# Kernel tuning notes

Measured on AMD Instinct MI355X. Metric: run time of the kernel, lower is better.

Reference implementation:

```python
import jax, jax.numpy as jnp
import numpy as np

H, W, CIN = 448, 608, 64
D = (128, 128, 1024)  # depth list from the module
SCALE = 0.02

def setup_inputs() -> dict:
    key = jax.random.key(0)
    ks = jax.random.split(key, 9)
    f32 = jnp.float32
    return {
        "x":  jax.random.normal(ks[0], (1, CIN, H, W), f32),
        "w1": jax.random.normal(ks[1], (D[0], CIN, 3, 3), f32) * SCALE,
        "b1": jax.random.normal(ks[2], (D[0],), f32) * SCALE,
        "w2": jax.random.normal(ks[3], (H, D[1], D[0]), f32) * SCALE,
        "b2": jax.random.normal(ks[4], (H, D[1]), f32) * SCALE,
        "w3": jax.random.normal(ks[5], (H, D[2], D[1]), f32) * SCALE,
        "b3": jax.random.normal(ks[6], (H, D[2]), f32) * SCALE,
        "w4": jax.random.normal(ks[7], (H, 2, D[2]), f32) * SCALE,
        "b4": jax.random.normal(ks[8], (H, 2), f32) * SCALE,
    }

def _lrelu(v):
    return jax.nn.leaky_relu(v, 0.01)  # PyTorch F.leaky_relu default slope

def reference(x, w1, b1, w2, b2, w3, b3, w4, b4):
    # stage_1: 3x3 conv, padding=1, + leaky_relu   -> [B,128,H,W]
    y = jax.lax.conv_general_dilated(
        x, w1, window_strides=(1, 1), padding='SAME',
        dimension_numbers=('NCHW', 'OIHW', 'NCHW'))
    y = _lrelu(y + b1[None, :, None, None])
    # transpose(1,2) + reshape -> grouped 1x1 convs (groups=H) == per-row GEMMs
    y = jnp.transpose(y, (0, 2, 1, 3))                      # [B,H,128,W]
    y = _lrelu(jnp.einsum('bhcw,hdc->bhdw', y, w2) + b2[None, :, :, None])
    y = _lrelu(jnp.einsum('bhcw,hdc->bhdw', y, w3) + b3[None, :, :, None])
    y = jnp.einsum('bhcw,hdc->bhdw', y, w4) + b4[None, :, :, None]  # [B,H,2,W]
    y = jnp.transpose(y, (0, 2, 1, 3))                      # [B,2,H,W]
    out = y[:, 0]
    mask = _lrelu(y[:, 1])   # mask branch      [B,H,W]
    return (out, mask)
```

## Files before the change

kernel.cpp:

```cpp
#include <hip/hip_runtime.h>

#define HH 448
#define WW 608
#define D1 128
#define D2 128
#define D3 1024
#define HWPROD (HH*WW)
#define CLW 164

typedef __bf16 bf16x8 __attribute__((ext_vector_type(8)));
typedef float  f32x4  __attribute__((ext_vector_type(4)));

__device__ inline unsigned short f2bf(float v) {
    __bf16 b = (__bf16)v;
    return __builtin_bit_cast(unsigned short, b);
}

__device__ inline bf16x8 cvt8c(const float* __restrict__ p) {
    f32x4 f0 = *reinterpret_cast<const f32x4*>(p);
    f32x4 f1 = *reinterpret_cast<const f32x4*>(p + 4);
    bf16x8 r;
    r[0]=(__bf16)f0[0]; r[1]=(__bf16)f0[1]; r[2]=(__bf16)f0[2]; r[3]=(__bf16)f0[3];
    r[4]=(__bf16)f1[0]; r[5]=(__bf16)f1[1]; r[6]=(__bf16)f1[2]; r[7]=(__bf16)f1[3];
    return r;
}

__global__ __launch_bounds__(256) void transpose_x_kernel(
    const float* __restrict__ x, unsigned short* __restrict__ xt)
{
    const int pos = blockIdx.x * 256 + threadIdx.x;
    #pragma unroll
    for (int c8 = 0; c8 < 8; ++c8) {
        bf16x8 r;
        #pragma unroll
        for (int j = 0; j < 8; ++j)
            r[j] = (__bf16)x[(size_t)(c8 * 8 + j) * HWPROD + pos];
        *reinterpret_cast<bf16x8*>(xt + (size_t)pos * 64 + c8 * 8) = r;
    }
}

__global__ __launch_bounds__(256) void convert_w1_kernel(
    const float* __restrict__ w1, unsigned short* __restrict__ w1t)
{
    const int idx = blockIdx.x * 256 + threadIdx.x;
    if (idx >= 9 * D1 * 64) return;
    const int tap = idx / (D1 * 64);
    const int rem = idx - tap * (D1 * 64);
    const int d = rem >> 6, c = rem & 63;
    w1t[idx] = f2bf(w1[(d * 64 + c) * 9 + tap]);
}

__global__ __launch_bounds__(512) void conv_kernel(
    const unsigned short* __restrict__ xt, const unsigned short* __restrict__ w1t,
    const float* __restrict__ b1, unsigned short* __restrict__ y1)
{
    __shared__ __align__(16) unsigned char lds[3 * CLW * 128];
    const int h      = blockIdx.y;
    const int wstart = blockIdx.x * 152;
    const int tid  = threadIdx.x;
    const int lane = tid & 63, wv = tid >> 6;
    const int l15 = lane & 15, lg = lane >> 4;
    const int wd = wv >> 2, wn = wv & 3;
    const int d0 = wd * 64;
    const int start = (wn < 2) ? wn * 3 : 6 + (wn - 2) * 2;
    const int cnt   = (wn < 2) ? 3 : 2;

    for (int i = 0; i < 8; ++i) {
        const int s = i * 512 + tid;
        if (s < 3 * CLW * 8) {
            const int slot = s & 7;
            const int rw   = s >> 3;
            const int ri   = rw / CLW;
            const int wl   = rw - ri * CLW;
            const int hs   = h + ri - 1;
            const int gw   = wstart + wl - 1;
            uint4 val = {0u, 0u, 0u, 0u};
            if ((unsigned)hs < (unsigned)HH && (unsigned)gw < (unsigned)WW)
                val = *reinterpret_cast<const uint4*>(xt + ((size_t)hs * WW + gw) * 64 + slot * 8);
            const int dslot = slot ^ (rw & 7);
            *reinterpret_cast<uint4*>(&lds[(size_t)rw * 128 + dslot * 16]) = val;
        }
    }
    __syncthreads();

    f32x4 acc[3][4] = {};

    #pragma unroll
    for (int tap = 0; tap < 9; ++tap) {
        const int ty = tap / 3, tx = tap - ty * 3;
        bf16x8 a[4][2];
        #pragma unroll
        for (int mf = 0; mf < 4; ++mf)
            #pragma unroll
            for (int kc = 0; kc < 2; ++kc)
                a[mf][kc] = *reinterpret_cast<const bf16x8*>(
                    w1t + ((size_t)(tap * D1 + d0 + mf * 16 + l15)) * 64 + kc * 32 + lg * 8);
        #pragma unroll
        for (int f = 0; f < 3; ++f) {
            if (f < cnt) {
                const int col = (start + f) * 16 + l15;
                const int row = ty * CLW + col + tx;
                bf16x8 b[2];
                #pragma unroll
                for (int kc = 0; kc < 2; ++kc) {
                    const int sl = (kc * 4 + lg) ^ (row & 7);
                    b[kc] = *reinterpret_cast<const bf16x8*>(&lds[(size_t)row * 128 + sl * 16]);
                }
                #pragma unroll
                for (int mf = 0; mf < 4; ++mf)
                    #pragma unroll
                    for (int kc = 0; kc < 2; ++kc)
                        acc[f][mf] = __builtin_amdgcn_mfma_f32_16x16x32_bf16(
                            a[mf][kc], b[kc], acc[f][mf], 0, 0, 0);
            }
        }
    }

    f32x4 b1v[4];
    #pragma unroll
    for (int mf = 0; mf < 4; ++mf)
        b1v[mf] = *reinterpret_cast<const f32x4*>(b1 + d0 + mf * 16 + lg * 4);

    #pragma unroll
    for (int f = 0; f < 3; ++f) {
        if (f < cnt) {
            const int wl = (start + f) * 16 + l15;
            if (wl < 152) {
                const int w = wstart + wl;
                #pragma unroll
                for (int mf = 0; mf < 4; ++mf) {
                    ushort4 o;
                    #pragma unroll
                    for (int r = 0; r < 4; ++r) {
                        float v = acc[f][mf][r] + b1v[mf][r];
                        v = fmaxf(v, 0.01f * v);
                        ((unsigned short*)&o)[r] = f2bf(v);
                    }
                    *reinterpret_cast<ushort4*>(
                        y1 + ((size_t)h * WW + w) * D1 + d0 + mf * 16 + lg * 4) = o;
                }
            }
        }
    }
}

__device__ inline void decode_pair(int bid, int& h, int& half) {
    const int s = bid & 7, j = bid >> 3;
    half = j & 1;
    h = (j >> 1) * 8 + s;
}

__global__ __launch_bounds__(512) void gemm2_kernel(
    const unsigned short* __restrict__ y1, const float* __restrict__ w2,
    const float* __restrict__ b2, unsigned short* __restrict__ y2)
{
    __shared__ __align__(16) unsigned char lds[304 * 256];
    int h, half;
    decode_pair(blockIdx.x, h, half);
    const int wstart = half * 304;
    const int tid = threadIdx.x;
    const int lane = tid & 63, wv = tid >> 6;
    const int l15 = lane & 15, lg = lane >> 4;
    const int e0 = wv * 16;

    {
        const unsigned char* src = reinterpret_cast<const unsigned char*>(
            y1 + ((size_t)h * WW + wstart) * D1);
        #pragma unroll
        for (int i = 0; i < 10; ++i) {
            const int c16 = i * 512 + tid;
            if (c16 < 304 * 16) {
                const int byte = c16 * 16;
                const int row  = byte >> 8;
                const int slot = (byte >> 4) & 15;
                uint4 val = *reinterpret_cast<const uint4*>(src + byte);
                *reinterpret_cast<uint4*>(&lds[row * 256 + ((slot ^ (row & 15)) << 4)]) = val;
            }
        }
    }

    bf16x8 a[4];
    #pragma unroll
    for (int kc = 0; kc < 4; ++kc)
        a[kc] = cvt8c(w2 + ((size_t)h * D2 + e0 + l15) * D1 + kc * 32 + lg * 8);
    f32x4 b2v = *reinterpret_cast<const f32x4*>(b2 + (size_t)h * D2 + e0 + lg * 4);

    __syncthreads();

    for (int nf = 0; nf < 19; ++nf) {
        const int wl = nf * 16 + l15;
        bf16x8 b[4];
        #pragma unroll
        for (int kc = 0; kc < 4; ++kc) {
            const int sl = (kc * 4 + lg) ^ (wl & 15);
            b[kc] = *reinterpret_cast<const bf16x8*>(&lds[(size_t)wl * 256 + sl * 16]);
        }
        f32x4 t = {};
        #pragma unroll
        for (int kc = 0; kc < 4; ++kc)
            t = __builtin_amdgcn_mfma_f32_16x16x32_bf16(a[kc], b[kc], t, 0, 0, 0);
        ushort4 o;
        #pragma unroll
        for (int r = 0; r < 4; ++r) {
            float v = t[r] + b2v[r];
            v = fmaxf(v, 0.01f * v);
            ((unsigned short*)&o)[r] = f2bf(v);
        }
        *reinterpret_cast<ushort4*>(
            y2 + ((size_t)h * WW + wstart + wl) * D2 + e0 + lg * 4) = o;
    }
}

__global__ __launch_bounds__(512) void gemm3_kernel(
    const unsigned short* __restrict__ y2, const float* __restrict__ w3,
    const float* __restrict__ b3, const float* __restrict__ w4,
    const float* __restrict__ b4, float* __restrict__ out)
{
    __shared__ __align__(16) unsigned char lds[304 * 256 + 2 * 304 * 4];
    float* pk = reinterpret_cast<float*>(&lds[304 * 256]);
    int h, half;
    decode_pair(blockIdx.x, h, half);
    const int wstart = half * 304;
    const int tid = threadIdx.x;
    const int lane = tid & 63, wv = tid >> 6;
    const int l15 = lane & 15, lg = lane >> 4;
    const int e0 = wv * 128;

    for (int i = tid; i < 2 * 304; i += 512) pk[i] = 0.f;

    {
        const unsigned char* src = reinterpret_cast<const unsigned char*>(
            y2 + ((size_t)h * WW + wstart) * D2);
        #pragma unroll
        for (int i = 0; i < 10; ++i) {
            const int c16 = i * 512 + tid;
            if (c16 < 304 * 16) {
                const int byte = c16 * 16;
                const int row  = byte >> 8;
                const int slot = (byte >> 4) & 15;
                uint4 val = *reinterpret_cast<const uint4*>(src + byte);
                *reinterpret_cast<uint4*>(&lds[row * 256 + ((slot ^ (row & 15)) << 4)]) = val;
            }
        }
    }
    __syncthreads();

    for (int ct = 0; ct < 4; ++ct) {
        const int e32 = e0 + ct * 32;
        bf16x8 a[2][4];
        #pragma unroll
        for (int mf = 0; mf < 2; ++mf)
            #pragma unroll
            for (int kc = 0; kc < 4; ++kc)
                a[mf][kc] = cvt8c(w3 + ((size_t)h * D3 + e32 + mf * 16 + l15) * D2 + kc * 32 + lg * 8);
        f32x4 b3v[2], w40[2], w41[2];
        #pragma unroll
        for (int mf = 0; mf < 2; ++mf) {
            b3v[mf] = *reinterpret_cast<const f32x4*>(b3 + (size_t)h * D3 + e32 + mf * 16 + lg * 4);
            w40[mf] = *reinterpret_cast<const f32x4*>(w4 + (size_t)h * 2 * D3 + e32 + mf * 16 + lg * 4);
            w41[mf] = *reinterpret_cast<const f32x4*>(w4 + (size_t)h * 2 * D3 + D3 + e32 + mf * 16 + lg * 4);
        }

        for (int nf = 0; nf < 19; ++nf) {
            const int wl = nf * 16 + l15;
            bf16x8 b[4];
            #pragma unroll
            for (int kc = 0; kc < 4; ++kc) {
                const int sl = (kc * 4 + lg) ^ (wl & 15);
                b[kc] = *reinterpret_cast<const bf16x8*>(&lds[(size_t)wl * 256 + sl * 16]);
            }
            float p0 = 0.f, p1 = 0.f;
            #pragma unroll
            for (int mf = 0; mf < 2; ++mf) {
                f32x4 t = {};
                #pragma unroll
                for (int kc = 0; kc < 4; ++kc)
                    t = __builtin_amdgcn_mfma_f32_16x16x32_bf16(a[mf][kc], b[kc], t, 0, 0, 0);
                #pragma unroll
                for (int r = 0; r < 4; ++r) {
                    float v = t[r] + b3v[mf][r];
                    v = fmaxf(v, 0.01f * v);
                    p0 = fmaf(w40[mf][r], v, p0);
                    p1 = fmaf(w41[mf][r], v, p1);
                }
            }
            p0 += __shfl_xor(p0, 16); p0 += __shfl_xor(p0, 32);
            p1 += __shfl_xor(p1, 16); p1 += __shfl_xor(p1, 32);
            if (lane < 16) {
                atomicAdd(&pk[wl], p0);
                atomicAdd(&pk[304 + wl], p1);
            }
        }
    }
    __syncthreads();

    const float bb0 = b4[h * 2 + 0], bb1 = b4[h * 2 + 1];
    for (int i = tid; i < 304; i += 512) {
        float s0 = pk[i] + bb0;
        float s1 = pk[304 + i] + bb1;
        out[(size_t)h * WW + wstart + i] = s0;
        out[(size_t)HWPROD + (size_t)h * WW + wstart + i] = fmaxf(s1, 0.01f * s1);
    }
}

extern "C" void kernel_launch(void* const* d_in, const int* in_sizes, int n_in,
                              void* d_out, int out_size, void* d_ws, size_t ws_size,
                              hipStream_t stream) {
    const float* x  = (const float*)d_in[0];
    const float* w1 = (const float*)d_in[1];
    const float* b1 = (const float*)d_in[2];
    const float* w2 = (const float*)d_in[3];
    const float* b2 = (const float*)d_in[4];
    const float* w3 = (const float*)d_in[5];
    const float* b3 = (const float*)d_in[6];
    const float* w4 = (const float*)d_in[7];
    const float* b4 = (const float*)d_in[8];
    float* out = (float*)d_out;

    char* ws = (char*)d_ws;
    size_t off = 0;
    unsigned short* y1 = (unsigned short*)(ws + off); off += (size_t)HWPROD * D1 * 2;
    char* regionB = ws + off; off += (size_t)HWPROD * D2 * 2;
    unsigned short* xt = (unsigned short*)regionB;
    unsigned short* y2 = (unsigned short*)regionB;
    unsigned short* w1t = (unsigned short*)(ws + off); off += (size_t)9 * D1 * 64 * 2;

    transpose_x_kernel<<<HWPROD / 256, 256, 0, stream>>>(x, xt);
    convert_w1_kernel<<<(9 * D1 * 64 + 255) / 256, 256, 0, stream>>>(w1, w1t);

    conv_kernel <<<dim3(4, HH), 512, 0, stream>>>(xt, w1t, b1, y1);
    gemm2_kernel<<<896, 512, 0, stream>>>(y1, w2, b2, y2);
    gemm3_kernel<<<896, 512, 0, stream>>>(y2, w3, b3, w4, b4, out);
}
```

Before: 368.2 us.

## Split gemm3 into quarter-row tiles, accumulate partials in registers, fold bias into accumulator

gemm3 now splits each row into four column tiles of 160 columns (the last has 128), which doubles the grid and shrinks the LDS footprint per block. Per-column partial dot products are kept in registers across the four channel tiles, and the shuffle reduction plus LDS atomics run once at the end instead of every iteration. All three kernels now initialize the MFMA accumulators with the bias, and the swizzled LDS offsets are precomputed. The costs are higher register pressure from the 20 partial accumulators and reloading the w3 tiles in twice as many blocks.

```diff
diff --git a/kernel.cpp b/kernel.cpp
--- a/kernel.cpp
+++ b/kernel.cpp
@@ -81,9 +81,19 @@
             *reinterpret_cast<uint4*>(&lds[(size_t)rw * 128 + dslot * 16]) = val;
         }
     }
-    __syncthreads();
-
-    f32x4 acc[3][4] = {};
+
+    f32x4 b1v[4];
+    #pragma unroll
+    for (int mf = 0; mf < 4; ++mf)
+        b1v[mf] = *reinterpret_cast<const f32x4*>(b1 + d0 + mf * 16 + lg * 4);
+    f32x4 acc[3][4];
+    #pragma unroll
+    for (int f = 0; f < 3; ++f)
+        #pragma unroll
+        for (int mf = 0; mf < 4; ++mf)
+            acc[f][mf] = b1v[mf];
+
+    __syncthreads();
 
     #pragma unroll
     for (int tap = 0; tap < 9; ++tap) {
@@ -116,11 +126,6 @@
         }
     }
 
-    f32x4 b1v[4];
-    #pragma unroll
-    for (int mf = 0; mf < 4; ++mf)
-        b1v[mf] = *reinterpret_cast<const f32x4*>(b1 + d0 + mf * 16 + lg * 4);
-
     #pragma unroll
     for (int f = 0; f < 3; ++f) {
         if (f < cnt) {
@@ -132,7 +137,7 @@
                     ushort4 o;
                     #pragma unroll
                     for (int r = 0; r < 4; ++r) {
-                        float v = acc[f][mf][r] + b1v[mf][r];
+                        float v = acc[f][mf][r];
                         v = fmaxf(v, 0.01f * v);
                         ((unsigned short*)&o)[r] = f2bf(v);
                     }
@@ -185,29 +190,29 @@
         a[kc] = cvt8c(w2 + ((size_t)h * D2 + e0 + l15) * D1 + kc * 32 + lg * 8);
     f32x4 b2v = *reinterpret_cast<const f32x4*>(b2 + (size_t)h * D2 + e0 + lg * 4);
 
+    int boff[4];
+    #pragma unroll
+    for (int kc = 0; kc < 4; ++kc)
+        boff[kc] = l15 * 256 + (((kc * 4 + lg) ^ l15) << 4);
+
     __syncthreads();
 
     for (int nf = 0; nf < 19; ++nf) {
-        const int wl = nf * 16 + l15;
-        bf16x8 b[4];
+        f32x4 t = b2v;
         #pragma unroll
         for (int kc = 0; kc < 4; ++kc) {
-            const int sl = (kc * 4 + lg) ^ (wl & 15);
-            b[kc] = *reinterpret_cast<const bf16x8*>(&lds[(size_t)wl * 256 + sl * 16]);
-        }
-        f32x4 t = {};
-        #pragma unroll
-        for (int kc = 0; kc < 4; ++kc)
-            t = __builtin_amdgcn_mfma_f32_16x16x32_bf16(a[kc], b[kc], t, 0, 0, 0);
+            bf16x8 b = *reinterpret_cast<const bf16x8*>(&lds[nf * 4096 + boff[kc]]);
+            t = __builtin_amdgcn_mfma_f32_16x16x32_bf16(a[kc], b, t, 0, 0, 0);
+        }
         ushort4 o;
         #pragma unroll
         for (int r = 0; r < 4; ++r) {
-            float v = t[r] + b2v[r];
+            float v = t[r];
             v = fmaxf(v, 0.01f * v);
             ((unsigned short*)&o)[r] = f2bf(v);
         }
         *reinterpret_cast<ushort4*>(
-            y2 + ((size_t)h * WW + wstart + wl) * D2 + e0 + lg * 4) = o;
+            y2 + ((size_t)h * WW + wstart + nf * 16 + l15) * D2 + e0 + lg * 4) = o;
     }
 }
 
@@ -216,25 +221,24 @@
     const float* __restrict__ b3, const float* __restrict__ w4,
     const float* __restrict__ b4, float* __restrict__ out)
 {
-    __shared__ __align__(16) unsigned char lds[304 * 256 + 2 * 304 * 4];
-    float* pk = reinterpret_cast<float*>(&lds[304 * 256]);
-    int h, half;
-    decode_pair(blockIdx.x, h, half);
-    const int wstart = half * 304;
+    __shared__ __align__(16) unsigned char lds[160 * 256];
+    int h, q;
+    { const int s = blockIdx.x & 7, j = blockIdx.x >> 3; q = j & 3; h = (j >> 2) * 8 + s; }
+    const int wstart = q * 160;
+    const int cols = (q < 3) ? 160 : 128;
+    const int nfc = cols >> 4;
     const int tid = threadIdx.x;
     const int lane = tid & 63, wv = tid >> 6;
     const int l15 = lane & 15, lg = lane >> 4;
     const int e0 = wv * 128;
 
-    for (int i = tid; i < 2 * 304; i += 512) pk[i] = 0.f;
-
     {
         const unsigned char* src = reinterpret_cast<const unsigned char*>(
             y2 + ((size_t)h * WW + wstart) * D2);
         #pragma unroll
-        for (int i = 0; i < 10; ++i) {
+        for (int i = 0; i < 5; ++i) {
             const int c16 = i * 512 + tid;
-            if (c16 < 304 * 16) {
+            if (c16 < cols * 16) {
                 const int byte = c16 * 16;
                 const int row  = byte >> 8;
                 const int slot = (byte >> 4) & 15;
@@ -243,6 +247,16 @@
             }
         }
     }
+
+    int boff[4];
+    #pragma unroll
+    for (int kc = 0; kc < 4; ++kc)
+        boff[kc] = l15 * 256 + (((kc * 4 + lg) ^ l15) << 4);
+
+    float pacc0[10], pacc1[10];
+    #pragma unroll
+    for (int i = 0; i < 10; ++i) { pacc0[i] = 0.f; pacc1[i] = 0.f; }
+
     __syncthreads();
 
     for (int ct = 0; ct < 4; ++ct) {
@@ -261,45 +275,57 @@
             w41[mf] = *reinterpret_cast<const f32x4*>(w4 + (size_t)h * 2 * D3 + D3 + e32 + mf * 16 + lg * 4);
         }
 
-        for (int nf = 0; nf < 19; ++nf) {
-            const int wl = nf * 16 + l15;
-            bf16x8 b[4];
-            #pragma unroll
-            for (int kc = 0; kc < 4; ++kc) {
-                const int sl = (kc * 4 + lg) ^ (wl & 15);
-                b[kc] = *reinterpret_cast<const bf16x8*>(&lds[(size_t)wl * 256 + sl * 16]);
-            }
-            float p0 = 0.f, p1 = 0.f;
-            #pragma unroll
-            for (int mf = 0; mf < 2; ++mf) {
-                f32x4 t = {};
-                #pragma unroll
-                for (int kc = 0; kc < 4; ++kc)
-                    t = __builtin_amdgcn_mfma_f32_16x16x32_bf16(a[mf][kc], b[kc], t, 0, 0, 0);
+        #pragma unroll
+        for (int nf = 0; nf < 10; ++nf) {
+            if (nf < nfc) {
+                f32x4 t0 = b3v[0], t1 = b3v[1];
+                #pragma unroll
+                for (int kc = 0; kc < 4; ++kc) {
+                    bf16x8 b = *reinterpret_cast<const bf16x8*>(&lds[nf * 4096 + boff[kc]]);
+                    t0 = __builtin_amdgcn_mfma_f32_16x16x32_bf16(a[0][kc], b, t0, 0, 0, 0);
+                    t1 = __builtin_amdgcn_mfma_f32_16x16x32_bf16(a[1][kc], b, t1, 0, 0, 0);
+                }
+                float p0 = 0.f, p1 = 0.f;
                 #pragma unroll
                 for (int r = 0; r < 4; ++r) {
-                    float v = t[r] + b3v[mf][r];
-                    v = fmaxf(v, 0.01f * v);
-                    p0 = fmaf(w40[mf][r], v, p0);
-                    p1 = fmaf(w41[mf][r], v, p1);
+                    float v0 = fmaxf(t0[r], 0.01f * t0[r]);
+                    float v1 = fmaxf(t1[r], 0.01f * t1[r]);
+                    p0 = fmaf(w40[0][r], v0, p0);
+                    p0 = fmaf(w40[1][r], v1, p0);
+                    p1 = fmaf(w41[0][r], v0, p1);
+                    p1 = fmaf(w41[1][r], v1, p1);
                 }
-            }
+                pacc0[nf] += p0;
+                pacc1[nf] += p1;
+            }
+        }
+    }
+
+    __syncthreads();
+    float* pk = reinterpret_cast<float*>(lds);
+    for (int i = tid; i < 2 * 160; i += 512) pk[i] = 0.f;
+    __syncthreads();
+
+    #pragma unroll
+    for (int nf = 0; nf < 10; ++nf) {
+        if (nf < nfc) {
+            float p0 = pacc0[nf], p1 = pacc1[nf];
             p0 += __shfl_xor(p0, 16); p0 += __shfl_xor(p0, 32);
             p1 += __shfl_xor(p1, 16); p1 += __shfl_xor(p1, 32);
             if (lane < 16) {
-                atomicAdd(&pk[wl], p0);
-                atomicAdd(&pk[304 + wl], p1);
+                atomicAdd(&pk[nf * 16 + l15], p0);
+                atomicAdd(&pk[160 + nf * 16 + l15], p1);
             }
         }
     }
     __syncthreads();
 
     const float bb0 = b4[h * 2 + 0], bb1 = b4[h * 2 + 1];
-    for (int i = tid; i < 304; i += 512) {
-        float s0 = pk[i] + bb0;
-        float s1 = pk[304 + i] + bb1;
-        out[(size_t)h * WW + wstart + i] = s0;
-        out[(size_t)HWPROD + (size_t)h * WW + wstart + i] = fmaxf(s1, 0.01f * s1);
+    if (tid < cols) {
+        float s0 = pk[tid] + bb0;
+        float s1 = pk[160 + tid] + bb1;
+        out[(size_t)h * WW + wstart + tid] = s0;
+        out[(size_t)HWPROD + (size_t)h * WW + wstart + tid] = fmaxf(s1, 0.01f * s1);
     }
 }
 
@@ -330,5 +356,5 @@
 
     conv_kernel <<<dim3(4, HH), 512, 0, stream>>>(xt, w1t, b1, y1);
     gemm2_kernel<<<896, 512, 0, stream>>>(y1, w2, b2, y2);
-    gemm3_kernel<<<896, 512, 0, stream>>>(y2, w3, b3, w4, b4, out);
-}
+    gemm3_kernel<<<448 * 4, 512, 0, stream>>>(y2, w3, b3, w4, b4, out);
+}
```

Result: slower. 381.7 us (+3.7%).

## Retile GEMM2/GEMM3 waves and reduce final projection with an f16 MFMA

Applied to the files above, without the earlier changes.

GEMM3 now gives each wave 64-row weight tiles processed in two chunks instead of four 32-row chunks. It replaces the per-lane FMA dot product with w4 plus the cross-lane shuffles by a 16x16x16 f16 MFMA that multiplies the activations by w4 padded to 16 rows. GEMM2 gives each wave 32 output rows over half the columns, so each B-fragment load feeds two MFMAs. Biases are preloaded into the accumulators in conv1, GEMM2 and GEMM3. This cuts LDS reads and shuffle/ALU work per MFMA, at the cost of more registers and of the final reduction running in f16 precision.

```diff
diff --git a/kernel.cpp b/kernel.cpp
--- a/kernel.cpp
+++ b/kernel.cpp
@@ -10,6 +10,7 @@
 
 typedef __bf16 bf16x8 __attribute__((ext_vector_type(8)));
 typedef float  f32x4  __attribute__((ext_vector_type(4)));
+typedef _Float16 f16x4 __attribute__((ext_vector_type(4)));
 
 __device__ inline unsigned short f2bf(float v) {
     __bf16 b = (__bf16)v;
@@ -81,9 +82,19 @@
             *reinterpret_cast<uint4*>(&lds[(size_t)rw * 128 + dslot * 16]) = val;
         }
     }
+
+    f32x4 b1v[4];
+    #pragma unroll
+    for (int mf = 0; mf < 4; ++mf)
+        b1v[mf] = *reinterpret_cast<const f32x4*>(b1 + d0 + mf * 16 + lg * 4);
+    f32x4 acc[3][4];
+    #pragma unroll
+    for (int f = 0; f < 3; ++f)
+        #pragma unroll
+        for (int mf = 0; mf < 4; ++mf)
+            acc[f][mf] = b1v[mf];
+
     __syncthreads();
-
-    f32x4 acc[3][4] = {};
 
     #pragma unroll
     for (int tap = 0; tap < 9; ++tap) {
@@ -116,11 +127,6 @@
         }
     }
 
-    f32x4 b1v[4];
-    #pragma unroll
-    for (int mf = 0; mf < 4; ++mf)
-        b1v[mf] = *reinterpret_cast<const f32x4*>(b1 + d0 + mf * 16 + lg * 4);
-
     #pragma unroll
     for (int f = 0; f < 3; ++f) {
         if (f < cnt) {
@@ -132,7 +138,7 @@
                     ushort4 o;
                     #pragma unroll
                     for (int r = 0; r < 4; ++r) {
-                        float v = acc[f][mf][r] + b1v[mf][r];
+                        float v = acc[f][mf][r];
                         v = fmaxf(v, 0.01f * v);
                         ((unsigned short*)&o)[r] = f2bf(v);
                     }
@@ -154,14 +160,15 @@
     const unsigned short* __restrict__ y1, const float* __restrict__ w2,
     const float* __restrict__ b2, unsigned short* __restrict__ y2)
 {
-    __shared__ __align__(16) unsigned char lds[304 * 256];
+    __shared__ __align__(16) unsigned char lds[312 * 256];
     int h, half;
     decode_pair(blockIdx.x, h, half);
     const int wstart = half * 304;
     const int tid = threadIdx.x;
     const int lane = tid & 63, wv = tid >> 6;
     const int l15 = lane & 15, lg = lane >> 4;
-    const int e0 = wv * 16;
+    const int rw = (wv & 3) * 32;
+    const int cs = (wv >> 2) * 152;
 
     {
         const unsigned char* src = reinterpret_cast<const unsigned char*>(
@@ -179,35 +186,51 @@
         }
     }
 
-    bf16x8 a[4];
+    bf16x8 a[2][4];
+    #pragma unroll
+    for (int mf = 0; mf < 2; ++mf)
+        #pragma unroll
+        for (int kc = 0; kc < 4; ++kc)
+            a[mf][kc] = cvt8c(w2 + ((size_t)h * D2 + rw + mf * 16 + l15) * D1 + kc * 32 + lg * 8);
+    f32x4 b2v[2];
+    #pragma unroll
+    for (int mf = 0; mf < 2; ++mf)
+        b2v[mf] = *reinterpret_cast<const f32x4*>(b2 + (size_t)h * D2 + rw + mf * 16 + lg * 4);
+
+    const int csw = (cs + l15) & 15;
+    int boff[4];
     #pragma unroll
     for (int kc = 0; kc < 4; ++kc)
-        a[kc] = cvt8c(w2 + ((size_t)h * D2 + e0 + l15) * D1 + kc * 32 + lg * 8);
-    f32x4 b2v = *reinterpret_cast<const f32x4*>(b2 + (size_t)h * D2 + e0 + lg * 4);
+        boff[kc] = ((kc * 4 + lg) ^ csw) << 4;
 
     __syncthreads();
 
-    for (int nf = 0; nf < 19; ++nf) {
-        const int wl = nf * 16 + l15;
+    for (int nf = 0; nf < 10; ++nf) {
+        const int col = cs + nf * 16 + l15;
         bf16x8 b[4];
         #pragma unroll
+        for (int kc = 0; kc < 4; ++kc)
+            b[kc] = *reinterpret_cast<const bf16x8*>(&lds[col * 256 + boff[kc]]);
+        f32x4 t[2] = {b2v[0], b2v[1]};
+        #pragma unroll
         for (int kc = 0; kc < 4; ++kc) {
-            const int sl = (kc * 4 + lg) ^ (wl & 15);
-            b[kc] = *reinterpret_cast<const bf16x8*>(&lds[(size_t)wl * 256 + sl * 16]);
-        }
-        f32x4 t = {};
-        #pragma unroll
-        for (int kc = 0; kc < 4; ++kc)
-            t = __builtin_amdgcn_mfma_f32_16x16x32_bf16(a[kc], b[kc], t, 0, 0, 0);
-        ushort4 o;
-        #pragma unroll
-        for (int r = 0; r < 4; ++r) {
-            float v = t[r] + b2v[r];
-            v = fmaxf(v, 0.01f * v);
-            ((unsigned short*)&o)[r] = f2bf(v);
-        }
-        *reinterpret_cast<ushort4*>(
-            y2 + ((size_t)h * WW + wstart + wl) * D2 + e0 + lg * 4) = o;
+            t[0] = __builtin_amdgcn_mfma_f32_16x16x32_bf16(a[0][kc], b[kc], t[0], 0, 0, 0);
+            t[1] = __builtin_amdgcn_mfma_f32_16x16x32_bf16(a[1][kc], b[kc], t[1], 0, 0, 0);
+        }
+        if (col < cs + 152) {
+            #pragma unroll
+            for (int mf = 0; mf < 2; ++mf) {
+                ushort4 o;
+                #pragma unroll
+                for (int r = 0; r < 4; ++r) {
+                    float v = t[mf][r];
+                    v = fmaxf(v, 0.01f * v);
+                    ((unsigned short*)&o)[r] = f2bf(v);
+                }
+                *reinterpret_cast<ushort4*>(
+                    y2 + ((size_t)h * WW + wstart + col) * D2 + rw + mf * 16 + lg * 4) = o;
+            }
+        }
     }
 }
 
@@ -243,63 +266,94 @@
             }
         }
     }
+
+    int boff[4];
+    #pragma unroll
+    for (int kc = 0; kc < 4; ++kc)
+        boff[kc] = l15 * 256 + (((kc * 4 + lg) ^ l15) << 4);
+
+    bf16x8 a[4][4];
+    f32x4 b3v[4];
+    f16x4 af[4];
+    {
+        const int e64 = e0;
+        #pragma unroll
+        for (int mf = 0; mf < 4; ++mf) {
+            #pragma unroll
+            for (int kc = 0; kc < 4; ++kc)
+                a[mf][kc] = cvt8c(w3 + ((size_t)h * D3 + e64 + mf * 16 + l15) * D2 + kc * 32 + lg * 8);
+            b3v[mf] = *reinterpret_cast<const f32x4*>(b3 + (size_t)h * D3 + e64 + mf * 16 + lg * 4);
+            f16x4 z = {(_Float16)0.f, (_Float16)0.f, (_Float16)0.f, (_Float16)0.f};
+            if (l15 < 2) {
+                f32x4 wv4 = *reinterpret_cast<const f32x4*>(
+                    w4 + (size_t)h * 2 * D3 + (size_t)l15 * D3 + e64 + mf * 16 + lg * 4);
+                #pragma unroll
+                for (int j = 0; j < 4; ++j) z[j] = (_Float16)wv4[j];
+            }
+            af[mf] = z;
+        }
+    }
+
     __syncthreads();
 
-    for (int ct = 0; ct < 4; ++ct) {
-        const int e32 = e0 + ct * 32;
-        bf16x8 a[2][4];
-        #pragma unroll
-        for (int mf = 0; mf < 2; ++mf)
+    #pragma unroll 1
+    for (int ct = 0; ct < 2; ++ct) {
+        if (ct == 1) {
+            const int e64 = e0 + 64;
+            #pragma unroll
+            for (int mf = 0; mf < 4; ++mf) {
+                #pragma unroll
+                for (int kc = 0; kc < 4; ++kc)
+                    a[mf][kc] = cvt8c(w3 + ((size_t)h * D3 + e64 + mf * 16 + l15) * D2 + kc * 32 + lg * 8);
+                b3v[mf] = *reinterpret_cast<const f32x4*>(b3 + (size_t)h * D3 + e64 + mf * 16 + lg * 4);
+                f16x4 z = {(_Float16)0.f, (_Float16)0.f, (_Float16)0.f, (_Float16)0.f};
+                if (l15 < 2) {
+                    f32x4 wv4 = *reinterpret_cast<const f32x4*>(
+                        w4 + (size_t)h * 2 * D3 + (size_t)l15 * D3 + e64 + mf * 16 + lg * 4);
+                    #pragma unroll
+                    for (int j = 0; j < 4; ++j) z[j] = (_Float16)wv4[j];
+                }
+                af[mf] = z;
+            }
+        }
+
+        for (int nf = 0; nf < 19; ++nf) {
+            bf16x8 b[4];
             #pragma unroll
             for (int kc = 0; kc < 4; ++kc)
-                a[mf][kc] = cvt8c(w3 + ((size_t)h * D3 + e32 + mf * 16 + l15) * D2 + kc * 32 + lg * 8);
-        f32x4 b3v[2], w40[2], w41[2];
-        #pragma unroll
-        for (int mf = 0; mf < 2; ++mf) {
-            b3v[mf] = *reinterpret_cast<const f32x4*>(b3 + (size_t)h * D3 + e32 + mf * 16 + lg * 4);
-            w40[mf] = *reinterpret_cast<const f32x4*>(w4 + (size_t)h * 2 * D3 + e32 + mf * 16 + lg * 4);
-            w41[mf] = *reinterpret_cast<const f32x4*>(w4 + (size_t)h * 2 * D3 + D3 + e32 + mf * 16 + lg * 4);
-        }
-
-        for (int nf = 0; nf < 19; ++nf) {
-            const int wl = nf * 16 + l15;
-            bf16x8 b[4];
-            #pragma unroll
-            for (int kc = 0; kc < 4; ++kc) {
-                const int sl = (kc * 4 + lg) ^ (wl & 15);
-                b[kc] = *reinterpret_cast<const bf16x8*>(&lds[(size_t)wl * 256 + sl * 16]);
-            }
-            float p0 = 0.f, p1 = 0.f;
-            #pragma unroll
-            for (int mf = 0; mf < 2; ++mf) {
-                f32x4 t = {};
-                #pragma unroll
-                for (int kc = 0; kc < 4; ++kc)
-                    t = __builtin_amdgcn_mfma_f32_16x16x32_bf16(a[mf][kc], b[kc], t, 0, 0, 0);
+                b[kc] = *reinterpret_cast<const bf16x8*>(&lds[nf * 4096 + boff[kc]]);
+            f32x4 t[4] = {b3v[0], b3v[1], b3v[2], b3v[3]};
+            #pragma unroll
+            for (int kc = 0; kc < 4; ++kc)
+                #pragma unroll
+                for (int mf = 0; mf < 4; ++mf)
+                    t[mf] = __builtin_amdgcn_mfma_f32_16x16x32_bf16(a[mf][kc], b[kc], t[mf], 0, 0, 0);
+
+            f32x4 pacc = {};
+            #pragma unroll
+            for (int mf = 0; mf < 4; ++mf) {
+                f16x4 vb;
                 #pragma unroll
                 for (int r = 0; r < 4; ++r) {
-                    float v = t[r] + b3v[mf][r];
-                    v = fmaxf(v, 0.01f * v);
-                    p0 = fmaf(w40[mf][r], v, p0);
-                    p1 = fmaf(w41[mf][r], v, p1);
-                }
-            }
-            p0 += __shfl_xor(p0, 16); p0 += __shfl_xor(p0, 32);
-            p1 += __shfl_xor(p1, 16); p1 += __shfl_xor(p1, 32);
-            if (lane < 16) {
-                atomicAdd(&pk[wl], p0);
-                atomicAdd(&pk[304 + wl], p1);
+                    float v = fmaxf(t[mf][r], 0.01f * t[mf][r]);
+                    vb[r] = (_Float16)v;
+                }
+                pacc = __builtin_amdgcn_mfma_f32_16x16x16f16(af[mf], vb, pacc, 0, 0, 0);
+            }
+            if (lg == 0) {
+                atomicAdd(&pk[nf * 16 + l15], pacc[0]);
+                atomicAdd(&pk[304 + nf * 16 + l15], pacc[1]);
             }
         }
     }
     __syncthreads();
 
     const float bb0 = b4[h * 2 + 0], bb1 = b4[h * 2 + 1];
-    for (int i = tid; i < 304; i += 512) {
-        float s0 = pk[i] + bb0;
-        float s1 = pk[304 + i] + bb1;
-        out[(size_t)h * WW + wstart + i] = s0;
-        out[(size_t)HWPROD + (size_t)h * WW + wstart + i] = fmaxf(s1, 0.01f * s1);
+    if (tid < 304) {
+        float s0 = pk[tid] + bb0;
+        float s1 = pk[304 + tid] + bb1;
+        out[(size_t)h * WW + wstart + tid] = s0;
+        out[(size_t)HWPROD + (size_t)h * WW + wstart + tid] = fmaxf(s1, 0.01f * s1);
     }
 }
 
```

After: 361.9 us. Within noise of the previous version (-1.7%).
